# Kernel tuning notes

Hardware: AMD Instinct MI355X
Metric: run time of the kernel (lower is better)

The kernel has to match this reference:

```python
import jax, jax.numpy as jnp
import numpy as np

# Dims: B samples, D=2048 backbone feature dim (resnet50 fc.in_features),
B, D, G, R, K, C = 16384, 2048, 8, 6, 3, 16


def setup_inputs() -> dict:
    key = jax.random.key(0)
    k0, k1, k2, k3 = jax.random.split(key, 4)
    feats = jax.random.normal(k0, (B, D), dtype=jnp.float32)          # backbone output (dropout=eval identity)
    roi_ids = jax.random.randint(k1, (B,), 0, G)                       # per-sample routing id (roi_names)
    W_reg = jax.random.normal(k2, (G, R, D), dtype=jnp.float32) * 0.02  # reg_heads[roi].weight
    b_reg = jnp.zeros((G, R), dtype=jnp.float32)                       # reg_heads[roi].bias
    W_cls = jax.random.normal(k3, (G, K, C, D), dtype=jnp.float32) * 0.02  # cls_heads[roi][k].weight
    b_cls = jnp.zeros((G, K, C), dtype=jnp.float32)                    # cls_heads[roi][k].bias
    return {"feats": feats, "roi_ids": roi_ids, "W_reg": W_reg, "b_reg": b_reg,
            "W_cls": W_cls, "b_cls": b_cls}


def reference(feats, roi_ids, W_reg, b_reg, W_cls, b_cls):
    # Original loop applies, per sample i, the Linear heads of roi_names[i].
    # Vectorized: compute all-ROI head outputs densely, then gather the routed one.
    # (Same math per sample; dropout is identity in eval mode.)
    reg_all = jnp.einsum('bd,grd->bgr', feats, W_reg) + b_reg[None]        # [B, G, R]
    cls_all = jnp.einsum('bd,gkcd->bgkc', feats, W_cls) + b_cls[None]      # [B, G, K, C]
    reg = jnp.take_along_axis(reg_all, roi_ids[:, None, None], axis=1)[:, 0]            # [B, R]
    cls = jnp.take_along_axis(cls_all, roi_ids[:, None, None, None], axis=1)[:, 0]      # [B, K, C]
    return reg, cls
```

## Files before the change

### kernel.cpp

```cpp
#include <hip/hip_runtime.h>
#include <hip/hip_bf16.h>

#define NB   16384
#define ND   2048
#define NG   8
#define NR   6
#define NKC  48
#define NOUT 54
#define LROW 136
#define BM   32
#define KC   128
#define NCH  (ND / KC)
#define MAXT (NB / BM + NG)

typedef __attribute__((ext_vector_type(8))) short short8_t;
typedef __attribute__((ext_vector_type(4))) float f32x4;

__device__ __forceinline__ unsigned short f2bf(float x) {
    union { float f; unsigned u; } v; v.f = x;
    unsigned r = v.u + 0x7FFFu + ((v.u >> 16) & 1u);
    return (unsigned short)(r >> 16);
}

__device__ __forceinline__ short8_t cvt8(float4 a, float4 b) {
    short8_t s;
    s[0] = (short)f2bf(a.x); s[1] = (short)f2bf(a.y);
    s[2] = (short)f2bf(a.z); s[3] = (short)f2bf(a.w);
    s[4] = (short)f2bf(b.x); s[5] = (short)f2bf(b.y);
    s[6] = (short)f2bf(b.z); s[7] = (short)f2bf(b.w);
    return s;
}

__device__ __forceinline__ void gl_lds16(const void* g, void* s) {
    __builtin_amdgcn_global_load_lds(
        (const __attribute__((address_space(1))) void*)g,
        (__attribute__((address_space(3))) void*)s,
        16, 0, 0);
}

#define WAITV(N) do { asm volatile("s_waitcnt vmcnt(" #N ")" ::: "memory"); \
                      __builtin_amdgcn_sched_barrier(0); } while (0)
#define BAR() do { __builtin_amdgcn_s_barrier(); \
                   __builtin_amdgcn_sched_barrier(0); } while (0)

__global__ void hist_kernel(const int* __restrict__ roi, int* __restrict__ counts) {
    int i = blockIdx.x * 256 + threadIdx.x;
    int g = roi[i];
    int lane = threadIdx.x & 63;
    #pragma unroll
    for (int gg = 0; gg < NG; ++gg) {
        unsigned long long m = __ballot(g == gg);
        if (m && lane == (int)(__ffsll((unsigned long long)m) - 1))
            atomicAdd(&counts[gg], (int)__popcll(m));
    }
}

__global__ void scatter_kernel(const int* __restrict__ roi, const int* __restrict__ counts,
                               int* __restrict__ ranks, int* __restrict__ perm) {
    int off[NG];
    int acc = 0;
    #pragma unroll
    for (int gg = 0; gg < NG; ++gg) { off[gg] = acc; acc += counts[gg]; }
    int i = blockIdx.x * 256 + threadIdx.x;
    int g = roi[i];
    int lane = threadIdx.x & 63;
    #pragma unroll
    for (int gg = 0; gg < NG; ++gg) {
        unsigned long long m = __ballot(g == gg);
        if (!m) continue;
        int leader = (int)(__ffsll((unsigned long long)m) - 1);
        int base = 0;
        if (lane == leader) base = atomicAdd(&ranks[gg], (int)__popcll(m));
        base = __shfl(base, leader);
        if (g == gg) {
            int rank = (int)__popcll(m & ((1ull << lane) - 1ull));
            perm[off[gg] + base + rank] = i;
        }
    }
}

__global__ void prep_kernel(const int* __restrict__ roi, int* __restrict__ cnt,
                            int* __restrict__ perm,
                            const float* __restrict__ Wreg, const float* __restrict__ Wcls,
                            short* __restrict__ Wbf) {
    if (blockIdx.x < 64) {
        int i = blockIdx.x * 256 + threadIdx.x;
        int g = roi[i];
        int lane = threadIdx.x & 63;
        #pragma unroll
        for (int gg = 0; gg < NG; ++gg) {
            unsigned long long m = __ballot(g == gg);
            if (!m) continue;
            int leader = (int)(__ffsll((unsigned long long)m) - 1);
            int base = 0;
            if (lane == leader) base = atomicAdd(&cnt[gg], (int)__popcll(m));
            base = __shfl(base, leader);
            if (g == gg) {
                int rank = (int)__popcll(m & ((1ull << lane) - 1ull));
                perm[gg * NB + base + rank] = i;
            }
        }
    } else {
        int u = (blockIdx.x - 64) * 256 + threadIdx.x;
        int l = u & 63;
        int q = (u >> 6) & 7;
        int c = (u >> 9) & 31;
        int g = u >> 14;
        int nh = q >> 2, nf = (q >> 1) & 1, ks = q & 1;
        int row = nh * 32 + nf * 16 + (l & 15);
        int k   = c * 64 + ks * 32 + (l >> 4) * 8;
        short8_t v = {0, 0, 0, 0, 0, 0, 0, 0};
        if (row < NOUT) {
            const float* s = (row < NR) ? Wreg + (size_t)(g * NR + row) * ND + k
                                        : Wcls + (size_t)(g * NKC + row - NR) * ND + k;
            float4 a = *(const float4*)s;
            float4 b = *(const float4*)(s + 4);
            v = cvt8(a, b);
        }
        *(short8_t*)(Wbf + (size_t)u * 8) = v;
    }
}

__launch_bounds__(512, 4)
__global__ void gemm_q_kernel(const float* __restrict__ feats,
                              const short* __restrict__ Wbf,
                              const float* __restrict__ breg, const float* __restrict__ bcls,
                              const int* __restrict__ cnt, const int* __restrict__ perm,
                              int* __restrict__ qhead, float* __restrict__ out) {
    __shared__ __align__(16) char lds[3][24576];
    __shared__ int sRow[64];
    __shared__ int sTile;

    int tid = threadIdx.x, w = tid >> 6, l = tid & 63, lr = l & 15, lq = l >> 4;
    int mt = w >> 1, nh = w & 1;

    int ts[NG + 1]; ts[0] = 0;
    #pragma unroll
    for (int gg = 0; gg < NG; ++gg) ts[gg + 1] = ts[gg] + ((cnt[gg] + 63) >> 6);
    const int Ttot = ts[NG];

    const int key   = lr & 7;
    const int rbyt  = mt * 4096 + lr * 256;
    const int o00 = (((lq * 2 + 0) ^ key) << 4);
    const int o01 = (((lq * 2 + 1) ^ key) << 4);
    const int o10 = (((8 + lq * 2 + 0) ^ key) << 4);
    const int o11 = (((8 + lq * 2 + 1) ^ key) << 4);
    const int r0 = (2 * w + 0) * 4 + lq;
    const int r1 = (2 * w + 1) * 4 + lq;
    const int sp0 = (((l & 15) ^ (r0 & 7)) << 4);
    const int sp1 = (((l & 15) ^ (r1 & 7)) << 4);
    const int B6 = NB * NR;

    for (;;) {
        if (tid == 0) sTile = atomicAdd(qhead, 1);
        __syncthreads();
        int t = sTile;
        if (t >= Ttot) break;

        int g = 0;
        #pragma unroll
        for (int gg = 0; gg < NG; ++gg) if (t >= ts[gg + 1]) g = gg + 1;
        int cg = cnt[g];
        int rbase = (t - ts[g]) * 64;
        int nv = cg - rbase; if (nv > 64) nv = 64;

        if (tid < 64) {
            int r = rbase + tid;
            if (r >= cg) r = cg - 1;
            sRow[tid] = perm[g * NB + r];
        }
        __syncthreads();

        const char* a0c = (const char*)(feats + (size_t)sRow[r0] * ND) + sp0;
        const char* a1c = (const char*)(feats + (size_t)sRow[r1] * ND) + sp1;
        const char* bB  = (const char*)Wbf + (size_t)g * 262144 + w * 1024 + l * 16;

#define STAGE(cc, sl) do {                                                     \
        size_t co_ = (size_t)(cc) * 256;                                       \
        gl_lds16(a0c + co_, &lds[sl][w * 2048]);                               \
        gl_lds16(a1c + co_, &lds[sl][w * 2048 + 1024]);                        \
        gl_lds16(bB + (size_t)(cc) * 8192, &lds[sl][16384 + w * 1024]);        \
    } while (0)

#define CSTEP(ks, o_0, o_1) do {                                               \
        const char* Ab_ = &lds[csl][0] + rbyt;                                 \
        const char* Bb_ = &lds[csl][16384] + nh * 4096 + (ks) * 1024 + l * 16; \
        float4 x0 = *(const float4*)(Ab_ + (ks) * 0 + o_0);                    \
        float4 x1 = *(const float4*)(Ab_ + o_1);                               \
        short8_t af = cvt8(x0, x1);                                            \
        short8_t b0 = *(const short8_t*)(Bb_);                                 \
        short8_t b1 = *(const short8_t*)(Bb_ + 2048);                          \
        acc0 = __builtin_amdgcn_mfma_f32_16x16x32_bf16(af, b0, acc0, 0, 0, 0); \
        acc1 = __builtin_amdgcn_mfma_f32_16x16x32_bf16(af, b1, acc1, 0, 0, 0); \
    } while (0)

        f32x4 acc0 = {0, 0, 0, 0}, acc1 = {0, 0, 0, 0};

        STAGE(0, 0); STAGE(1, 1);
        int csl = 0;
        #pragma unroll
        for (int c = 0; c < 32; ++c) {
            if (c + 2 < 32) STAGE(c + 2, (c + 2) % 3);
            if (c < 30)       WAITV(6);
            else if (c == 30) WAITV(3);
            else              WAITV(0);
            BAR();
            CSTEP(0, o00, o01);
            CSTEP(1, o10, o11);
            BAR();
            csl = (csl == 2) ? 0 : csl + 1;
        }
#undef STAGE
#undef CSTEP

        #pragma unroll
        for (int n = 0; n < 2; ++n) {
            f32x4 v = n ? acc1 : acc0;
            int col = nh * 32 + n * 16 + lr;
            if (col < NOUT) {
                #pragma unroll
                for (int j = 0; j < 4; ++j) {
                    int row = mt * 16 + lq * 4 + j;
                    if (row < nv) {
                        int smp = sRow[row];
                        if (col < NR) out[smp * NR + col] = v[j] + breg[g * NR + col];
                        else          out[B6 + smp * NKC + (col - NR)] = v[j] + bcls[g * NKC + (col - NR)];
                    }
                }
            }
        }
        __syncthreads();
    }
}

__launch_bounds__(256, 3)
__global__ void gemm_kernel(const float* __restrict__ feats,
                            const float* __restrict__ Wreg, const float* __restrict__ breg,
                            const float* __restrict__ Wcls, const float* __restrict__ bcls,
                            const int* __restrict__ counts, const int* __restrict__ perm,
                            float* __restrict__ out, int stride) {
    __shared__ __align__(16) short Bsh[2][64][LROW];
    __shared__ int sRow[BM];

    int ts[NG + 1]; ts[0] = 0;
    int off[NG]; int acc = 0;
    #pragma unroll
    for (int gg = 0; gg < NG; ++gg) {
        int c = counts[gg];
        off[gg] = stride ? gg * stride : acc;
        acc += c;
        ts[gg + 1] = ts[gg] + (c + BM - 1) / BM;
    }
    int b = blockIdx.x;
    if (b >= ts[NG]) return;
    int g = 0;
    #pragma unroll
    for (int gg = 0; gg < NG; ++gg) if (b >= ts[gg + 1]) g = gg + 1;
    int gcnt  = counts[g];
    int goff  = off[g];
    int rbase = (b - ts[g]) * BM;
    int nvalid = gcnt - rbase; if (nvalid > BM) nvalid = BM;

    int tid = threadIdx.x;
    if (tid < BM) {
        int r = rbase + tid;
        if (r >= gcnt) r = gcnt - 1;
        sRow[tid] = perm[goff + r];
    }
    __syncthreads();

    int rB = tid >> 2;
    int cq = tid & 3;
    const float* wsrc = nullptr;
    if (rB < NR)        wsrc = Wreg + ((size_t)g * NR + rB) * ND + cq * 32;
    else if (rB < NOUT) wsrc = Wcls + ((size_t)g * NKC + (rB - NR)) * ND + cq * 32;

    int w = tid >> 6, l = tid & 63, lr = l & 15, lq = l >> 4;
    int mt = w & 1, nh = w >> 1;
    const float* aptr = feats + (size_t)sRow[mt * 16 + lr] * ND + lq * 8;
    const short* brp = (const short*)&Bsh[0][0][0] + (nh * 32 + lr) * LROW + lq * 8;

    f32x4 acc0 = {0, 0, 0, 0}, acc1 = {0, 0, 0, 0};
    float4 rb[8];

    if (wsrc) {
        #pragma unroll
        for (int i = 0; i < 8; ++i) rb[i] = *(const float4*)(wsrc + 4 * i);
    } else {
        #pragma unroll
        for (int i = 0; i < 8; ++i) rb[i] = make_float4(0.f, 0.f, 0.f, 0.f);
    }
    {
        short* bw = &Bsh[0][rB][cq * 32];
        #pragma unroll
        for (int j = 0; j < 4; ++j) *(short8_t*)(bw + 8 * j) = cvt8(rb[2 * j], rb[2 * j + 1]);
    }
    __syncthreads();

    #pragma unroll
    for (int c = 0; c < NCH; ++c) {
        const int cur = c & 1, nxt = cur ^ 1;
        if (c + 1 < NCH && wsrc) {
            const float* s = wsrc + (c + 1) * KC;
            #pragma unroll
            for (int i = 0; i < 8; ++i) rb[i] = *(const float4*)(s + 4 * i);
        }
        const short* bp = brp + cur * (64 * LROW);
        const float* ap = aptr + c * KC;
        #pragma unroll
        for (int ks = 0; ks < 4; ++ks) {
            float4 a0 = *(const float4*)(ap + ks * 32);
            float4 a1 = *(const float4*)(ap + ks * 32 + 4);
            short8_t af = cvt8(a0, a1);
            short8_t b0 = *(const short8_t*)(bp + ks * 32);
            short8_t b1 = *(const short8_t*)(bp + 16 * LROW + ks * 32);
            acc0 = __builtin_amdgcn_mfma_f32_16x16x32_bf16(af, b0, acc0, 0, 0, 0);
            acc1 = __builtin_amdgcn_mfma_f32_16x16x32_bf16(af, b1, acc1, 0, 0, 0);
        }
        if (c + 1 < NCH && wsrc) {
            short* bw = &Bsh[nxt][rB][cq * 32];
            #pragma unroll
            for (int j = 0; j < 4; ++j) *(short8_t*)(bw + 8 * j) = cvt8(rb[2 * j], rb[2 * j + 1]);
        } else if (c + 1 < NCH) {
            short8_t z = {0,0,0,0,0,0,0,0};
            short* bw = &Bsh[nxt][rB][cq * 32];
            #pragma unroll
            for (int j = 0; j < 4; ++j) *(short8_t*)(bw + 8 * j) = z;
        }
        __syncthreads();
    }

    const int B6 = NB * NR;
    #pragma unroll
    for (int n = 0; n < 2; ++n) {
        f32x4 v = n ? acc1 : acc0;
        int col = nh * 32 + n * 16 + lr;
        if (col < NOUT) {
            #pragma unroll
            for (int j = 0; j < 4; ++j) {
                int row = mt * 16 + lq * 4 + j;
                if (row < nvalid) {
                    int smp = sRow[row];
                    if (col < NR) out[smp * NR + col] = v[j] + breg[g * NR + col];
                    else          out[B6 + smp * NKC + (col - NR)] = v[j] + bcls[g * NKC + (col - NR)];
                }
            }
        }
    }
}

__global__ void fallback_kernel(const float* __restrict__ feats, const int* __restrict__ roi,
                                const float* __restrict__ Wreg, const float* __restrict__ breg,
                                const float* __restrict__ Wcls, const float* __restrict__ bcls,
                                float* __restrict__ out) {
    int i = blockIdx.x;
    int lane = threadIdx.x;
    int g = roi[i];
    const float* frow = feats + (size_t)i * ND;
    float f[32];
    #pragma unroll
    for (int q = 0; q < 32; ++q) f[q] = frow[lane + 64 * q];
    for (int o = 0; o < NOUT; ++o) {
        const float* wrow = (o < NR) ? Wreg + ((size_t)g * NR + o) * ND
                                     : Wcls + ((size_t)g * NKC + (o - NR)) * ND;
        float p = 0.f;
        #pragma unroll
        for (int q = 0; q < 32; ++q) p += f[q] * wrow[lane + 64 * q];
        #pragma unroll
        for (int s = 32; s; s >>= 1) p += __shfl_xor(p, s);
        if (lane == 0) {
            if (o < NR) out[i * NR + o] = p + breg[g * NR + o];
            else        out[NB * NR + i * NKC + (o - NR)] = p + bcls[g * NKC + (o - NR)];
        }
    }
}

extern "C" void kernel_launch(void* const* d_in, const int* in_sizes, int n_in,
                              void* d_out, int out_size, void* d_ws, size_t ws_size,
                              hipStream_t stream) {
    const float* feats = (const float*)d_in[0];
    const int*   roi   = (const int*)d_in[1];
    const float* Wreg  = (const float*)d_in[2];
    const float* breg  = (const float*)d_in[3];
    const float* Wcls  = (const float*)d_in[4];
    const float* bcls  = (const float*)d_in[5];
    float* out = (float*)d_out;

    const size_t wbfBytes = (size_t)NG * 131072 * 2;
    const size_t need_t1 = wbfBytes + 256 + (size_t)NG * NB * 4;
    const size_t need_t3 = 256 + (size_t)NB * 4;

    if (ws_size >= need_t1) {
        short* Wbf = (short*)d_ws;
        int* cnt   = (int*)((char*)d_ws + wbfBytes);
        int* qhead = cnt + 8;
        int* perm  = cnt + 64;
        hipMemsetAsync(cnt, 0, 64, stream);
        prep_kernel<<<576, 256, 0, stream>>>(roi, cnt, perm, Wreg, Wcls, Wbf);
        gemm_q_kernel<<<512, 512, 0, stream>>>(feats, Wbf, breg, bcls, cnt, perm, qhead, out);
    } else if (ws_size >= need_t3) {
        int* counts = (int*)d_ws;
        int* ranks  = counts + 8;
        int* perm   = counts + 64;
        hipMemsetAsync(counts, 0, 16 * sizeof(int), stream);
        hist_kernel<<<NB / 256, 256, 0, stream>>>(roi, counts);
        scatter_kernel<<<NB / 256, 256, 0, stream>>>(roi, counts, ranks, perm);
        gemm_kernel<<<MAXT, 256, 0, stream>>>(feats, Wreg, breg, Wcls, bcls, counts, perm, out, 0);
    } else {
        fallback_kernel<<<NB, 64, 0, stream>>>(feats, roi, Wreg, breg, Wcls, bcls, out);
    }
}
```

Before: 69.74 us.

## Replace persistent 64-row queue GEMM with one-block-per-16-row tile grid

Swaps the persistent-block atomic work queue (512-thread blocks, 64-row tiles) for a static grid of 256-thread blocks that each handle one 16-row tile of a ROI group. Each wave now computes one 16-column N slice instead of two, and the prep kernel's weight layout is reordered to match. The aim is finer load balancing, smaller LDS use per block, and no atomic tile fetch. In exchange, each B weight chunk is reloaded for every 16 rows, so weight traffic rises about fourfold, and there are many more block launches.

```diff
diff --git a/kernel.cpp b/kernel.cpp
--- a/kernel.cpp
+++ b/kernel.cpp
@@ -2,11 +2,12 @@
 #include <hip/hip_bf16.h>
 
 #define NB   16384
+#define NG   8
 #define ND   2048
-#define NG   8
 #define NR   6
 #define NKC  48
 #define NOUT 54
+#define NT16 (NB / 16 + NG)
 #define LROW 136
 #define BM   32
 #define KC   128
@@ -106,8 +107,8 @@
         int q = (u >> 6) & 7;
         int c = (u >> 9) & 31;
         int g = u >> 14;
-        int nh = q >> 2, nf = (q >> 1) & 1, ks = q & 1;
-        int row = nh * 32 + nf * 16 + (l & 15);
+        int n = q >> 1, ks = q & 1;
+        int row = n * 16 + (l & 15);
         int k   = c * 64 + ks * 32 + (l >> 4) * 8;
         short8_t v = {0, 0, 0, 0, 0, 0, 0, 0};
         if (row < NOUT) {
@@ -121,115 +122,97 @@
     }
 }
 
-__launch_bounds__(512, 4)
-__global__ void gemm_q_kernel(const float* __restrict__ feats,
+__launch_bounds__(256, 4)
+__global__ void gemm16_kernel(const float* __restrict__ feats,
                               const short* __restrict__ Wbf,
                               const float* __restrict__ breg, const float* __restrict__ bcls,
                               const int* __restrict__ cnt, const int* __restrict__ perm,
-                              int* __restrict__ qhead, float* __restrict__ out) {
-    __shared__ __align__(16) char lds[3][24576];
-    __shared__ int sRow[64];
-    __shared__ int sTile;
+                              float* __restrict__ out) {
+    __shared__ __align__(16) char lds[3][12288];
+    __shared__ int sRow[16];
 
     int tid = threadIdx.x, w = tid >> 6, l = tid & 63, lr = l & 15, lq = l >> 4;
-    int mt = w >> 1, nh = w & 1;
 
     int ts[NG + 1]; ts[0] = 0;
     #pragma unroll
-    for (int gg = 0; gg < NG; ++gg) ts[gg + 1] = ts[gg] + ((cnt[gg] + 63) >> 6);
-    const int Ttot = ts[NG];
-
-    const int key   = lr & 7;
-    const int rbyt  = mt * 4096 + lr * 256;
-    const int o00 = (((lq * 2 + 0) ^ key) << 4);
-    const int o01 = (((lq * 2 + 1) ^ key) << 4);
-    const int o10 = (((8 + lq * 2 + 0) ^ key) << 4);
-    const int o11 = (((8 + lq * 2 + 1) ^ key) << 4);
-    const int r0 = (2 * w + 0) * 4 + lq;
-    const int r1 = (2 * w + 1) * 4 + lq;
-    const int sp0 = (((l & 15) ^ (r0 & 7)) << 4);
-    const int sp1 = (((l & 15) ^ (r1 & 7)) << 4);
+    for (int gg = 0; gg < NG; ++gg) ts[gg + 1] = ts[gg] + ((cnt[gg] + 15) >> 4);
+    int b = blockIdx.x;
+    if (b >= ts[NG]) return;
+    int g = 0;
+    #pragma unroll
+    for (int gg = 0; gg < NG; ++gg) if (b >= ts[gg + 1]) g = gg + 1;
+    int cg = cnt[g];
+    int rbase = (b - ts[g]) * 16;
+    int nv = cg - rbase; if (nv > 16) nv = 16;
+
+    if (tid < 16) {
+        int r = rbase + tid;
+        if (r >= cg) r = cg - 1;
+        sRow[tid] = perm[g * NB + r];
+    }
+    __syncthreads();
+
+    int srow = 4 * w + lq;
+    const char* aSrc = (const char*)(feats + (size_t)sRow[srow] * ND)
+                     + (((l & 15) ^ (srow & 7)) << 4);
+    const char* bSrc = (const char*)Wbf + (size_t)g * 262144 + (2 * w) * 1024 + l * 16;
+
+    const int key = lr & 7;
+    const int ra00 = lr * 256 + (((0 * 8 + lq * 2 + 0) ^ key) << 4);
+    const int ra01 = lr * 256 + (((0 * 8 + lq * 2 + 1) ^ key) << 4);
+    const int ra10 = lr * 256 + (((1 * 8 + lq * 2 + 0) ^ key) << 4);
+    const int ra11 = lr * 256 + (((1 * 8 + lq * 2 + 1) ^ key) << 4);
+    const int rb0  = 4096 + (2 * w + 0) * 1024 + l * 16;
+    const int rb1  = 4096 + (2 * w + 1) * 1024 + l * 16;
+
+#define STAGE(cc, sl) do {                                                     \
+        gl_lds16(aSrc + (size_t)(cc) * 256, &lds[sl][w * 1024]);               \
+        const char* b_ = bSrc + (size_t)(cc) * 8192;                           \
+        gl_lds16(b_,        &lds[sl][4096 + 2 * w * 1024]);                    \
+        gl_lds16(b_ + 1024, &lds[sl][4096 + 2 * w * 1024 + 1024]);             \
+    } while (0)
+
+    f32x4 acc = {0, 0, 0, 0};
+
+    STAGE(0, 0); STAGE(1, 1);
+    int csl = 0;
+    #pragma unroll
+    for (int c = 0; c < 32; ++c) {
+        if (c + 2 < 32) STAGE(c + 2, (c + 2) % 3);
+        if (c < 30)       WAITV(6);
+        else if (c == 30) WAITV(3);
+        else              WAITV(0);
+        BAR();
+        {
+            const char* s = &lds[csl][0];
+            float4 a0 = *(const float4*)(s + ra00);
+            float4 a1 = *(const float4*)(s + ra01);
+            short8_t af0 = cvt8(a0, a1);
+            short8_t b0  = *(const short8_t*)(s + rb0);
+            acc = __builtin_amdgcn_mfma_f32_16x16x32_bf16(af0, b0, acc, 0, 0, 0);
+            float4 a2 = *(const float4*)(s + ra10);
+            float4 a3 = *(const float4*)(s + ra11);
+            short8_t af1 = cvt8(a2, a3);
+            short8_t b1  = *(const short8_t*)(s + rb1);
+            acc = __builtin_amdgcn_mfma_f32_16x16x32_bf16(af1, b1, acc, 0, 0, 0);
+        }
+        BAR();
+        csl = (csl == 2) ? 0 : csl + 1;
+    }
+#undef STAGE
+
     const int B6 = NB * NR;
-
-    for (;;) {
-        if (tid == 0) sTile = atomicAdd(qhead, 1);
-        __syncthreads();
-        int t = sTile;
-        if (t >= Ttot) break;
-
-        int g = 0;
-        #pragma unroll
-        for (int gg = 0; gg < NG; ++gg) if (t >= ts[gg + 1]) g = gg + 1;
-        int cg = cnt[g];
-        int rbase = (t - ts[g]) * 64;
-        int nv = cg - rbase; if (nv > 64) nv = 64;
-
-        if (tid < 64) {
-            int r = rbase + tid;
-            if (r >= cg) r = cg - 1;
-            sRow[tid] = perm[g * NB + r];
-        }
-        __syncthreads();
-
-        const char* a0c = (const char*)(feats + (size_t)sRow[r0] * ND) + sp0;
-        const char* a1c = (const char*)(feats + (size_t)sRow[r1] * ND) + sp1;
-        const char* bB  = (const char*)Wbf + (size_t)g * 262144 + w * 1024 + l * 16;
-
-#define STAGE(cc, sl) do {                                                     \
-        size_t co_ = (size_t)(cc) * 256;                                       \
-        gl_lds16(a0c + co_, &lds[sl][w * 2048]);                               \
-        gl_lds16(a1c + co_, &lds[sl][w * 2048 + 1024]);                        \
-        gl_lds16(bB + (size_t)(cc) * 8192, &lds[sl][16384 + w * 1024]);        \
-    } while (0)
-
-#define CSTEP(ks, o_0, o_1) do {                                               \
-        const char* Ab_ = &lds[csl][0] + rbyt;                                 \
-        const char* Bb_ = &lds[csl][16384] + nh * 4096 + (ks) * 1024 + l * 16; \
-        float4 x0 = *(const float4*)(Ab_ + (ks) * 0 + o_0);                    \
-        float4 x1 = *(const float4*)(Ab_ + o_1);                               \
-        short8_t af = cvt8(x0, x1);                                            \
-        short8_t b0 = *(const short8_t*)(Bb_);                                 \
-        short8_t b1 = *(const short8_t*)(Bb_ + 2048);                          \
-        acc0 = __builtin_amdgcn_mfma_f32_16x16x32_bf16(af, b0, acc0, 0, 0, 0); \
-        acc1 = __builtin_amdgcn_mfma_f32_16x16x32_bf16(af, b1, acc1, 0, 0, 0); \
-    } while (0)
-
-        f32x4 acc0 = {0, 0, 0, 0}, acc1 = {0, 0, 0, 0};
-
-        STAGE(0, 0); STAGE(1, 1);
-        int csl = 0;
-        #pragma unroll
-        for (int c = 0; c < 32; ++c) {
-            if (c + 2 < 32) STAGE(c + 2, (c + 2) % 3);
-            if (c < 30)       WAITV(6);
-            else if (c == 30) WAITV(3);
-            else              WAITV(0);
-            BAR();
-            CSTEP(0, o00, o01);
-            CSTEP(1, o10, o11);
-            BAR();
-            csl = (csl == 2) ? 0 : csl + 1;
-        }
-#undef STAGE
-#undef CSTEP
-
-        #pragma unroll
-        for (int n = 0; n < 2; ++n) {
-            f32x4 v = n ? acc1 : acc0;
-            int col = nh * 32 + n * 16 + lr;
-            if (col < NOUT) {
-                #pragma unroll
-                for (int j = 0; j < 4; ++j) {
-                    int row = mt * 16 + lq * 4 + j;
-                    if (row < nv) {
-                        int smp = sRow[row];
-                        if (col < NR) out[smp * NR + col] = v[j] + breg[g * NR + col];
-                        else          out[B6 + smp * NKC + (col - NR)] = v[j] + bcls[g * NKC + (col - NR)];
-                    }
-                }
+    int col = w * 16 + lr;
+    if (col < NOUT) {
+        #pragma unroll
+        for (int j = 0; j < 4; ++j) {
+            int row = lq * 4 + j;
+            if (row < nv) {
+                int smp = sRow[row];
+                if (col < NR) out[smp * NR + col] = acc[j] + breg[g * NR + col];
+                else          out[B6 + smp * NKC + (col - NR)] = acc[j] + bcls[g * NKC + (col - NR)];
             }
         }
-        __syncthreads();
     }
 }
 
@@ -393,11 +376,10 @@
     if (ws_size >= need_t1) {
         short* Wbf = (short*)d_ws;
         int* cnt   = (int*)((char*)d_ws + wbfBytes);
-        int* qhead = cnt + 8;
         int* perm  = cnt + 64;
         hipMemsetAsync(cnt, 0, 64, stream);
         prep_kernel<<<576, 256, 0, stream>>>(roi, cnt, perm, Wreg, Wcls, Wbf);
-        gemm_q_kernel<<<512, 512, 0, stream>>>(feats, Wbf, breg, bcls, cnt, perm, qhead, out);
+        gemm16_kernel<<<NT16, 256, 0, stream>>>(feats, Wbf, breg, bcls, cnt, perm, out);
     } else if (ws_size >= need_t3) {
         int* counts = (int*)d_ws;
         int* ranks  = counts + 8;
```

Measured after the change: 73.81 us. 5.8% more time.
